# Performance work log

Measured on AMD Instinct MI355X. Metric: run time of the kernel, lower is better.

Reference implementation:

```python
import jax, jax.numpy as jnp
import numpy as np

D_MODEL = 1024
EXPAND = 2
HEADDIM = 64
D_STATE = 64
CHUNK = 64
D_INNER = EXPAND * D_MODEL          # 2048
NHEADS = D_INNER // HEADDIM         # 32
D_MLP = int(2.5 * D_MODEL)          # 2560
BATCH = 2
SEQLEN = 4096
PROJ = 2 * D_INNER + 2 * NHEADS * D_STATE + NHEADS + NHEADS * (D_STATE // 2)


def rmsnorm(x, w, eps=1e-5):
    return x * jax.lax.rsqrt(jnp.mean(x * x, axis=-1, keepdims=True) + eps) * w


def apply_rope(x, angles):
    x1 = x[..., 0::2]
    x2 = x[..., 1::2]
    c = jnp.cos(angles)
    s = jnp.sin(angles)
    ev = c * x1 - s * x2
    od = s * x1 + c * x2
    return jnp.stack([ev, od], axis=-1).reshape(x.shape)


def segsum(x):
    # x: (b,h,c,l) -> (b,h,c,l,l); [i,j] = sum_{j<k<=i} x_k (no -inf mask, as in source)
    T = x.shape[-1]
    xx = jnp.broadcast_to(x[..., :, None], x.shape + (T,))
    mask = jnp.tril(jnp.ones((T, T), dtype=bool), -1)
    xx = jnp.where(mask, xx, 0.0)
    return jnp.cumsum(xx, axis=-2)


def ssd(x, A, B, C, chunk):
    # x: (b,s,h,p), A: (b,s,h), B/C: (b,s,h,n); s % chunk == 0
    b, s, h, p = x.shape
    n = B.shape[-1]
    c = s // chunk
    x_c = x.reshape(b, c, chunk, h, p).transpose(0, 1, 3, 2, 4)  # (b,c,h,l,p)
    B_c = B.reshape(b, c, chunk, h, n).transpose(0, 1, 3, 2, 4)  # (b,c,h,l,n)
    C_c = C.reshape(b, c, chunk, h, n).transpose(0, 1, 3, 2, 4)
    A_c = A.reshape(b, c, chunk, h).transpose(0, 1, 3, 2)        # (b,c,h,l)
    A_cum = jnp.cumsum(A_c, axis=-1)
    L = jnp.exp(segsum(A_c.transpose(0, 2, 1, 3))).transpose(0, 2, 1, 3, 4)  # (b,c,h,l,l)
    Bx = jnp.einsum('bchln,bchlp->bchpn', B_c, x_c)
    Y_diag = jnp.einsum('bchln,bchls,bchpn->bchlp', C_c, L, Bx)
    decay_states = jnp.exp(A_cum[..., -1:] - A_cum)
    states = jnp.einsum('bchln,bchl,bchlp->bchpn', B_c, decay_states, x_c)  # (b,c,h,p,n)
    decay_chunk = jnp.exp(A_cum[..., -1])  # (b,c,h)
    h0 = jnp.zeros_like(states[:, 0])

    def step(carry, inp):
        dec, st = inp  # dec: (b,h), st: (b,h,p,n)
        carry = carry * dec[:, :, None, None] + st
        return carry, carry

    _, hs = jax.lax.scan(step, h0, (decay_chunk.transpose(1, 0, 2),
                                    states.transpose(1, 0, 2, 3, 4)))
    final_states = hs.transpose(1, 0, 2, 3, 4)  # (b,c,h,p,n)
    Y_off = jnp.einsum('bchln,bchpn,bchl->bchlp', C_c, final_states, jnp.exp(A_cum))
    Y = (Y_diag + Y_off).transpose(0, 1, 3, 2, 4).reshape(b, s, h * p)
    return Y


def setup_inputs() -> dict:
    key = jax.random.key(0)
    ks = jax.random.split(key, 12)
    sc = 0.02
    return {
        'x': jax.random.normal(ks[0], (BATCH, SEQLEN, D_MODEL), jnp.float32),
        'norm1_w': jnp.ones((D_MODEL,), jnp.float32),
        'norm2_w': jnp.ones((D_MODEL,), jnp.float32),
        'W_in': sc * jax.random.normal(ks[1], (D_MODEL, PROJ), jnp.float32),
        'W_out': sc * jax.random.normal(ks[2], (D_INNER, D_MODEL), jnp.float32),
        'A_log': jax.random.uniform(ks[3], (NHEADS,), jnp.float32, -4.0, -1.0),
        'D_param': jnp.ones((NHEADS,), jnp.float32),
        'dt_bias': jax.random.uniform(ks[4], (NHEADS,), jnp.float32, 0.001, 0.1),
        'B_bias': jnp.ones((1, NHEADS, D_STATE), jnp.float32),
        'C_bias': jnp.ones((1, NHEADS, D_STATE), jnp.float32),
        'Bn_w': jnp.ones((D_STATE,), jnp.float32),
        'Cn_w': jnp.ones((D_STATE,), jnp.float32),
        'Wg': sc * jax.random.normal(ks[5], (D_MODEL, D_MLP), jnp.float32),
        'Wu': sc * jax.random.normal(ks[6], (D_MODEL, D_MLP), jnp.float32),
        'Wd': sc * jax.random.normal(ks[7], (D_MLP, D_MODEL), jnp.float32),
    }


def reference(x, norm1_w, norm2_w, W_in, W_out, A_log, D_param, dt_bias,
              B_bias, C_bias, Bn_w, Cn_w, Wg, Wu, Wd):
    b, s, _ = x.shape
    h = rmsnorm(x, norm1_w)
    proj = h @ W_in
    i = 0
    z = proj[..., i:i + D_INNER]; i += D_INNER
    x_ssm = proj[..., i:i + D_INNER]; i += D_INNER
    B = proj[..., i:i + NHEADS * D_STATE].reshape(b, s, NHEADS, D_STATE); i += NHEADS * D_STATE
    C = proj[..., i:i + NHEADS * D_STATE].reshape(b, s, NHEADS, D_STATE); i += NHEADS * D_STATE
    dt = proj[..., i:i + NHEADS]; i += NHEADS
    theta = proj[..., i:].reshape(b, s, NHEADS, D_STATE // 2)
    dt = jax.nn.softplus(dt + dt_bias)                 # (b,s,h)
    A = -jnp.exp(A_log) * dt
    alpha = jnp.exp(A)
    gamma = (alpha - 1.0) / (A + 1e-6) * 0.5 + 1.0
    B = rmsnorm(B, Bn_w) + B_bias
    C = rmsnorm(C, Cn_w) + C_bias
    cum_theta = jnp.cumsum(dt[..., None] * theta, axis=1)
    B = apply_rope(B, cum_theta)
    C = apply_rope(C, cum_theta)
    x_ssm = x_ssm.reshape(b, s, NHEADS, HEADDIM)
    y = ssd(x_ssm * gamma[..., None], A, B, C, CHUNK)
    skip = jnp.broadcast_to((D_param * x_ssm.sum(-1))[..., None], x_ssm.shape)
    y = y + skip.reshape(b, s, -1)
    y = y * (z * jax.nn.sigmoid(z))
    y = y @ W_out
    x = x + y
    h2 = rmsnorm(x, norm2_w)
    g = h2 @ Wg
    x = x + ((g * jax.nn.sigmoid(g)) * (h2 @ Wu)) @ Wd
    return x
```

## Files before the change

kernel.cpp:

```cpp
#include <hip/hip_runtime.h>
#include <cstdint>
#include <cmath>


typedef __bf16 bf16;
typedef __bf16 bf16x2 __attribute__((ext_vector_type(2)));
typedef __bf16 bf16x4 __attribute__((ext_vector_type(4)));
typedef __bf16 bf16x8 __attribute__((ext_vector_type(8)));
typedef float fx4 __attribute__((ext_vector_type(4)));

#define DEV __device__ __forceinline__

#define OFF_PROJ    0ull
#define OFF_HHI     134217728ull
#define OFF_HLO     150994944ull
#define OFF_WTIN    167772160ull
#define OFF_WTHI    184549376ull
#define OFF_WTLO    186908672ull
#define OFF_PROJT   189267968ull
#define OFF_BX      189267968ull
#define OFF_STATES  222822400ull
#define OFF_WTOUT   222822400ull
#define OFF_WTGU    227016704ull
#define OFF_WTD     237502464ull
#define OFF_ABUF    256376832ull
#define OFF_XSUM    257425408ull
#define OFF_ROWSUM  258473984ull
#define OFF_EXPA    260571136ull
#define OFF_DCHUNK  262668288ull
#define OFF_GAMMA   262684672ull
#define WS_NEEDED   263733248ull

#define OFF_GU      0ull
#define OFF_MBF     83886080ull

DEV void async_copy16(void* lds, const void* gptr) {
  __builtin_amdgcn_global_load_lds(
      (const __attribute__((address_space(1))) unsigned int*)(gptr),
      (__attribute__((address_space(3))) unsigned int*)(lds),
      16, 0, 0);
}

DEV float warp_sum64(float v) {
  #pragma unroll
  for (int o = 32; o; o >>= 1) v += __shfl_xor(v, o);
  return v;
}

DEV float red16(float v) {
  v += __shfl_xor(v, 1); v += __shfl_xor(v, 2);
  v += __shfl_xor(v, 4); v += __shfl_xor(v, 8);
  return v;
}

DEV float softplus_f(float x) { return x > 20.f ? x : log1pf(expf(x)); }
DEV float sigmoid_f(float x) { return 1.f / (1.f + expf(-x)); }

__global__ __launch_bounds__(256) void transpose_cast(
    const float* __restrict__ src, int ld, int col0,
    bf16* __restrict__ dst, int R, int C)
{
  __shared__ float tile[32][33];
  const int c0 = blockIdx.x * 32, r0 = blockIdx.y * 32;
  const int tx = threadIdx.x & 31, ty = threadIdx.x >> 5;
  #pragma unroll
  for (int ii = 0; ii < 4; ++ii) {
    int i = ty + ii * 8;
    int c = c0 + tx;
    tile[i][tx] = (c < C) ? src[(size_t)(r0 + i) * ld + col0 + c] : 0.f;
  }
  __syncthreads();
  #pragma unroll
  for (int ii = 0; ii < 4; ++ii) {
    int i = ty + ii * 8;
    dst[(size_t)(c0 + i) * R + r0 + tx] = (bf16)tile[tx][i];
  }
}

__global__ __launch_bounds__(256) void transpose_cast_hilo(
    const float* __restrict__ src, int ld, int col0,
    bf16* __restrict__ dhi, bf16* __restrict__ dlo, int R, int C)
{
  __shared__ float tile[32][33];
  const int c0 = blockIdx.x * 32, r0 = blockIdx.y * 32;
  const int tx = threadIdx.x & 31, ty = threadIdx.x >> 5;
  #pragma unroll
  for (int ii = 0; ii < 4; ++ii) {
    int i = ty + ii * 8;
    int c = c0 + tx;
    tile[i][tx] = (c < C) ? src[(size_t)(r0 + i) * ld + col0 + c] : 0.f;
  }
  __syncthreads();
  #pragma unroll
  for (int ii = 0; ii < 4; ++ii) {
    int i = ty + ii * 8;
    float v = tile[tx][i];
    bf16 hi = (bf16)v;
    size_t o = (size_t)(c0 + i) * R + r0 + tx;
    dhi[o] = hi;
    dlo[o] = (bf16)(v - (float)hi);
  }
}

__global__ __launch_bounds__(256) void rmsnorm_kernel(
    const float* __restrict__ x, const float* __restrict__ w,
    bf16* __restrict__ hi, bf16* __restrict__ lo)
{
  __shared__ float red[4];
  const size_t row = blockIdx.x;
  const int tid = threadIdx.x;
  float4 v = ((const float4*)(x + row * 1024))[tid];
  float ss = v.x * v.x + v.y * v.y + v.z * v.z + v.w * v.w;
  ss = warp_sum64(ss);
  if ((tid & 63) == 0) red[tid >> 6] = ss;
  __syncthreads();
  float tot = red[0] + red[1] + red[2] + red[3];
  float s = rsqrtf(tot * (1.f / 1024.f) + 1e-5f);
  float4 wv = ((const float4*)w)[tid];
  float h0 = v.x * s * wv.x, h1 = v.y * s * wv.y, h2 = v.z * s * wv.z, h3 = v.w * s * wv.w;
  bf16x4 hv = { (bf16)h0, (bf16)h1, (bf16)h2, (bf16)h3 };
  *(bf16x4*)(hi + row * 1024 + tid * 4) = hv;
  if (lo) {
    bf16x4 lv = { (bf16)(h0 - (float)hv[0]), (bf16)(h1 - (float)hv[1]),
                  (bf16)(h2 - (float)hv[2]), (bf16)(h3 - (float)hv[3]) };
    *(bf16x4*)(lo + row * 1024 + tid * 4) = lv;
  }
}

template <int MODE>
__global__ __launch_bounds__(256) void gemm_bt(
    const bf16* A, const bf16* B, void* Cout, const float* resid,
    int K, int lda, int ldc)
{
  __shared__ bf16 As[128 * 64];
  __shared__ bf16 Bs[128 * 64];
  const int tid = threadIdx.x, wid = tid >> 6, lane = tid & 63;
  const int m0 = blockIdx.y * 128, n0 = blockIdx.x * 128;
  const int wm = (wid & 1) * 64, wn = (wid >> 1) * 64;
  fx4 acc[4][4];
  #pragma unroll
  for (int i = 0; i < 4; ++i)
    #pragma unroll
    for (int j = 0; j < 4; ++j) { fx4 z = {0.f, 0.f, 0.f, 0.f}; acc[i][j] = z; }

  const int srow = wid * 32 + (lane >> 3);
  const int slot = lane & 7;

  for (int k0 = 0; k0 < K; k0 += 64) {
    __syncthreads();
    #pragma unroll
    for (int i = 0; i < 4; ++i) {
      int m = srow + i * 8;
      int cA = ((slot ^ (m & 7)) * 8);
      async_copy16(&As[wid * 2048 + i * 512], A + (size_t)(m0 + m) * lda + k0 + cA);
    }
    #pragma unroll
    for (int i = 0; i < 4; ++i) {
      int n = srow + i * 8;
      int cB = ((slot ^ (n & 7)) * 8);
      async_copy16(&Bs[wid * 2048 + i * 512], B + (size_t)(n0 + n) * K + k0 + cB);
    }
    __syncthreads();
    #pragma unroll
    for (int kk = 0; kk < 2; ++kk) {
      bf16x8 af[4], bfr[4];
      #pragma unroll
      for (int i = 0; i < 4; ++i) {
        int mm = wm + i * 16 + (lane & 15);
        int sA = (kk * 4 + (lane >> 4)) ^ (mm & 7);
        af[i] = *(const bf16x8*)&As[mm * 64 + sA * 8];
        int nn = wn + i * 16 + (lane & 15);
        int sB = (kk * 4 + (lane >> 4)) ^ (nn & 7);
        bfr[i] = *(const bf16x8*)&Bs[nn * 64 + sB * 8];
      }
      #pragma unroll
      for (int i = 0; i < 4; ++i)
        #pragma unroll
        for (int j = 0; j < 4; ++j)
          acc[i][j] = __builtin_amdgcn_mfma_f32_16x16x32_bf16(af[i], bfr[j], acc[i][j], 0, 0, 0);
    }
  }
  const int r0 = (lane >> 4) * 4, cc = lane & 15;
  #pragma unroll
  for (int i = 0; i < 4; ++i) {
    #pragma unroll
    for (int j = 0; j < 4; ++j) {
      #pragma unroll
      for (int r = 0; r < 4; ++r) {
        int m = m0 + wm + i * 16 + r0 + r;
        int n = n0 + wn + j * 16 + cc;
        size_t off = (size_t)m * ldc + n;
        float v = acc[i][j][r];
        if (MODE == 1) ((bf16*)Cout)[off] = (bf16)v;
        else ((float*)Cout)[off] = v + resid[off];
      }
    }
  }
}

__global__ __launch_bounds__(256) void gemm_tail(
    const bf16* Ahi, const bf16* Alo, const bf16* Whi, const bf16* Wlo,
    float* Cout)
{
  __shared__ bf16 Ah[128 * 64], Al[128 * 64], Bh[128 * 64], Bl[128 * 64];
  const int tid = threadIdx.x, wid = tid >> 6, lane = tid & 63;
  const int m0 = blockIdx.y * 128, n0 = blockIdx.x * 128;
  const int wm = (wid & 1) * 64, wn = (wid >> 1) * 64;
  fx4 acc[4][4];
  #pragma unroll
  for (int i = 0; i < 4; ++i)
    #pragma unroll
    for (int j = 0; j < 4; ++j) { fx4 z = {0.f, 0.f, 0.f, 0.f}; acc[i][j] = z; }

  const int srow = wid * 32 + (lane >> 3);
  const int slot = lane & 7;

  for (int k0 = 0; k0 < 1024; k0 += 64) {
    __syncthreads();
    #pragma unroll
    for (int i = 0; i < 4; ++i) {
      int m = srow + i * 8;
      int cA = ((slot ^ (m & 7)) * 8);
      size_t ao = (size_t)(m0 + m) * 1024 + k0 + cA;
      async_copy16(&Ah[wid * 2048 + i * 512], Ahi + ao);
      async_copy16(&Al[wid * 2048 + i * 512], Alo + ao);
      int n = srow + i * 8;
      int cB = ((slot ^ (n & 7)) * 8);
      size_t bo = (size_t)(n0 + n) * 1024 + k0 + cB;
      async_copy16(&Bh[wid * 2048 + i * 512], Whi + bo);
      async_copy16(&Bl[wid * 2048 + i * 512], Wlo + bo);
    }
    __syncthreads();
    #pragma unroll
    for (int kk = 0; kk < 2; ++kk) {
      bf16x8 ah[4], al[4], bh[4], bl[4];
      #pragma unroll
      for (int i = 0; i < 4; ++i) {
        int mm = wm + i * 16 + (lane & 15);
        int sA = (kk * 4 + (lane >> 4)) ^ (mm & 7);
        ah[i] = *(const bf16x8*)&Ah[mm * 64 + sA * 8];
        al[i] = *(const bf16x8*)&Al[mm * 64 + sA * 8];
        int nn = wn + i * 16 + (lane & 15);
        int sB = (kk * 4 + (lane >> 4)) ^ (nn & 7);
        bh[i] = *(const bf16x8*)&Bh[nn * 64 + sB * 8];
        bl[i] = *(const bf16x8*)&Bl[nn * 64 + sB * 8];
      }
      #pragma unroll
      for (int i = 0; i < 4; ++i)
        #pragma unroll
        for (int j = 0; j < 4; ++j) {
          acc[i][j] = __builtin_amdgcn_mfma_f32_16x16x32_bf16(ah[i], bh[j], acc[i][j], 0, 0, 0);
          acc[i][j] = __builtin_amdgcn_mfma_f32_16x16x32_bf16(ah[i], bl[j], acc[i][j], 0, 0, 0);
          acc[i][j] = __builtin_amdgcn_mfma_f32_16x16x32_bf16(al[i], bh[j], acc[i][j], 0, 0, 0);
        }
    }
  }
  const int r0 = (lane >> 4) * 4, cc = lane & 15;
  #pragma unroll
  for (int i = 0; i < 4; ++i)
    #pragma unroll
    for (int j = 0; j < 4; ++j)
      #pragma unroll
      for (int r = 0; r < 4; ++r) {
        int m = m0 + wm + i * 16 + r0 + r;
        int n = n0 + wn + j * 16 + cc;
        Cout[(size_t)m * 1152 + n] = acc[i][j][r];
      }
}

__global__ __launch_bounds__(256) void dt_kernel(
    float* projT, const float* __restrict__ A_log, const float* __restrict__ dt_bias,
    float* __restrict__ a_buf, float* __restrict__ gamma_buf)
{
  const int idx = blockIdx.x * 256 + threadIdx.x;
  const int t = idx >> 5, h = idx & 31;
  float dtr = projT[(size_t)t * 1152 + h] + dt_bias[h];
  float dt = softplus_f(dtr);
  float a = -expf(A_log[h]) * dt;
  float alpha = expf(a);
  float gamma = (alpha - 1.f) / (a + 1e-6f) * 0.5f + 1.f;
  projT[(size_t)t * 1152 + h] = dt;
  a_buf[idx] = a;
  gamma_buf[idx] = gamma;
}

__global__ __launch_bounds__(256, 6) void gemm_proj(
    const bf16* A, const bf16* B, bf16* Cout,
    const float* __restrict__ gamma_buf, float* __restrict__ xsum,
    const float* __restrict__ Bn_w, const float* __restrict__ Cn_w,
    const float* __restrict__ B_bias, const float* __restrict__ C_bias)
{
  __shared__ bf16 As[128 * 64];
  __shared__ bf16 Bs[128 * 64];
  const int tid = threadIdx.x, wid = tid >> 6, lane = tid & 63;
  const int m0 = blockIdx.y * 128, n0 = blockIdx.x * 128;
  const int wm = (wid & 1) * 64, wn = (wid >> 1) * 64;
  fx4 acc[4][4];
  #pragma unroll
  for (int i = 0; i < 4; ++i)
    #pragma unroll
    for (int j = 0; j < 4; ++j) { fx4 z = {0.f, 0.f, 0.f, 0.f}; acc[i][j] = z; }

  const int srow = wid * 32 + (lane >> 3);
  const int slot = lane & 7;

  for (int k0 = 0; k0 < 1024; k0 += 64) {
    __syncthreads();
    #pragma unroll
    for (int i = 0; i < 4; ++i) {
      int m = srow + i * 8;
      int cA = ((slot ^ (m & 7)) * 8);
      async_copy16(&As[wid * 2048 + i * 512], A + (size_t)(m0 + m) * 1024 + k0 + cA);
    }
    #pragma unroll
    for (int i = 0; i < 4; ++i) {
      int n = srow + i * 8;
      int cB = ((slot ^ (n & 7)) * 8);
      async_copy16(&Bs[wid * 2048 + i * 512], B + (size_t)(n0 + n) * 1024 + k0 + cB);
    }
    __syncthreads();
    #pragma unroll
    for (int kk = 0; kk < 2; ++kk) {
      bf16x8 af[4], bfr[4];
      #pragma unroll
      for (int i = 0; i < 4; ++i) {
        int mm = wm + i * 16 + (lane & 15);
        int sA = (kk * 4 + (lane >> 4)) ^ (mm & 7);
        af[i] = *(const bf16x8*)&As[mm * 64 + sA * 8];
        int nn = wn + i * 16 + (lane & 15);
        int sB = (kk * 4 + (lane >> 4)) ^ (nn & 7);
        bfr[i] = *(const bf16x8*)&Bs[nn * 64 + sB * 8];
      }
      #pragma unroll
      for (int i = 0; i < 4; ++i)
        #pragma unroll
        for (int j = 0; j < 4; ++j)
          acc[i][j] = __builtin_amdgcn_mfma_f32_16x16x32_bf16(af[i], bfr[j], acc[i][j], 0, 0, 0);
    }
  }
  const int r0 = (lane >> 4) * 4, cc = lane & 15;
  const int reg = n0 >> 11;
  const int hh = ((n0 + wn) & 2047) >> 6;
  if (reg == 0) {
    #pragma unroll
    for (int i = 0; i < 4; ++i)
      #pragma unroll
      for (int j = 0; j < 4; ++j)
        #pragma unroll
        for (int r = 0; r < 4; ++r) {
          int m = m0 + wm + i * 16 + r0 + r;
          int n = n0 + wn + j * 16 + cc;
          Cout[(size_t)m * 8192 + n] = (bf16)acc[i][j][r];
        }
  } else if (reg == 1) {
    #pragma unroll
    for (int i = 0; i < 4; ++i)
      #pragma unroll
      for (int r = 0; r < 4; ++r) {
        float s = acc[i][0][r] + acc[i][1][r] + acc[i][2][r] + acc[i][3][r];
        s = red16(s);
        int m = m0 + wm + i * 16 + r0 + r;
        if (cc == 0) xsum[(size_t)m * 32 + hh] = s;
        float g = gamma_buf[(size_t)m * 32 + hh];
        #pragma unroll
        for (int j = 0; j < 4; ++j) {
          int n = n0 + wn + j * 16 + cc;
          Cout[(size_t)m * 8192 + n] = (bf16)(acc[i][j][r] * g);
        }
      }
  } else {
    const float* w = (reg == 2) ? Bn_w : Cn_w;
    const float* bias = (reg == 2) ? B_bias : C_bias;
    #pragma unroll
    for (int i = 0; i < 4; ++i)
      #pragma unroll
      for (int r = 0; r < 4; ++r) {
        float ss = acc[i][0][r] * acc[i][0][r] + acc[i][1][r] * acc[i][1][r]
                 + acc[i][2][r] * acc[i][2][r] + acc[i][3][r] * acc[i][3][r];
        ss = red16(ss);
        float sc = rsqrtf(ss * (1.f / 64.f) + 1e-5f);
        int m = m0 + wm + i * 16 + r0 + r;
        #pragma unroll
        for (int j = 0; j < 4; ++j) {
          int n = n0 + wn + j * 16 + cc;
          Cout[(size_t)m * 8192 + n] =
              (bf16)(acc[i][j][r] * sc * w[j * 16 + cc] + bias[hh * 64 + j * 16 + cc]);
        }
      }
  }
}

__global__ __launch_bounds__(256) void chunk_sum_kernel(
    const float* __restrict__ projT, float* __restrict__ S)
{
  __shared__ float lds[8 * 288];
  const int blk = blockIdx.x;
  const int hq = blockIdx.y;
  const size_t row0 = (size_t)blk * 64;
  const int tid = threadIdx.x;
  float s = 0.f;
  #pragma unroll 1
  for (int batch = 0; batch < 8; ++batch) {
    __syncthreads();
    const float* src = projT + (row0 + batch * 8) * 1152;
    #pragma unroll
    for (int i = 0; i < 9; ++i) {
      int idx = i * 256 + tid;
      int r = idx / 288, col = idx - r * 288;
      int gcol = (col < 32) ? col : (32 + hq * 256 + (col - 32));
      lds[idx] = src[r * 1152 + gcol];
    }
    __syncthreads();
    int hl = tid >> 5, d = tid & 31;
    #pragma unroll
    for (int r = 0; r < 8; ++r)
      s += lds[r * 288 + hq * 8 + hl] * lds[r * 288 + 32 + hl * 32 + d];
  }
  S[(size_t)blk * 1024 + hq * 256 + tid] = s;
}

__global__ __launch_bounds__(256) void rope_kernel(
    bf16* proj, const float* __restrict__ projT, const float* __restrict__ S)
{
  __shared__ float angs[64 * 33], angc[64 * 33];
  const int blk = blockIdx.x;
  const int b = blk >> 11, c = (blk >> 5) & 63, h = blk & 31;
  const size_t t0 = (size_t)b * 4096 + c * 64;
  const int w = threadIdx.x >> 6, lane = threadIdx.x & 63;
  const float* tr = projT + (t0 + lane) * 1152;
  float dtv = tr[h];
  const float* thp = tr + 32 + h * 32 + w * 8;
  float4 th0 = *(const float4*)thp;
  float4 th1 = *(const float4*)(thp + 4);
  const float* Sp = S + (size_t)(b * 64 + lane) * 1024 + h * 32 + w * 8;
  float4 S0 = *(const float4*)Sp;
  float4 S1 = *(const float4*)(Sp + 4);
  float th[8] = { th0.x, th0.y, th0.z, th0.w, th1.x, th1.y, th1.z, th1.w };
  float Sv[8] = { S0.x, S0.y, S0.z, S0.w, S1.x, S1.y, S1.z, S1.w };
  #pragma unroll 1
  for (int j = 0; j < 8; ++j) {
    int d = w * 8 + j;
    float sv = (lane < c) ? Sv[j] : 0.f;
    float off = warp_sum64(sv);
    float v = dtv * th[j];
    #pragma unroll
    for (int o = 1; o < 64; o <<= 1) { float u = __shfl_up(v, o); if (lane >= o) v += u; }
    float ang = off + v;
    float sn, cs;
    sincosf(ang, &sn, &cs);
    angs[lane * 33 + d] = sn;
    angc[lane * 33 + d] = cs;
  }
  __syncthreads();
  const int tt = threadIdx.x >> 2, q = threadIdx.x & 3;
  const size_t base = (t0 + tt) * 8192 + 4096 + h * 64 + q * 16;
  #pragma unroll
  for (int m = 0; m < 2; ++m) {
    bf16* p = proj + base + m * 2048;
    bf16x8 v0 = *(const bf16x8*)(p);
    bf16x8 v1 = *(const bf16x8*)(p + 8);
    bf16x8 r0, r1;
    #pragma unroll
    for (int pp = 0; pp < 4; ++pp) {
      int d = q * 8 + pp;
      float e1 = (float)v0[2 * pp], e2 = (float)v0[2 * pp + 1];
      float sn = angs[tt * 33 + d], cs = angc[tt * 33 + d];
      r0[2 * pp]     = (bf16)(cs * e1 - sn * e2);
      r0[2 * pp + 1] = (bf16)(sn * e1 + cs * e2);
    }
    #pragma unroll
    for (int pp = 0; pp < 4; ++pp) {
      int d = q * 8 + 4 + pp;
      float e1 = (float)v1[2 * pp], e2 = (float)v1[2 * pp + 1];
      float sn = angs[tt * 33 + d], cs = angc[tt * 33 + d];
      r1[2 * pp]     = (bf16)(cs * e1 - sn * e2);
      r1[2 * pp + 1] = (bf16)(sn * e1 + cs * e2);
    }
    *(bf16x8*)(p) = r0;
    *(bf16x8*)(p + 8) = r1;
  }
}

__global__ __launch_bounds__(256) void ssd1_kernel(
    const bf16* __restrict__ proj, const float* __restrict__ a_buf,
    bf16* __restrict__ Bx, bf16* __restrict__ states,
    float* __restrict__ rowsum, float* __restrict__ expac, float* __restrict__ dchunk)
{
  __shared__ bf16 Xs[64 * 72], Bs[64 * 72];
  __shared__ float acum[64], dsv[64];
  const int blk = blockIdx.x;
  const int h = blk & 31;
  const size_t bs0 = ((size_t)(blk >> 5)) * 64;
  const int tid = threadIdx.x;
  const int l = tid >> 2, p0 = (tid & 3) * 16;
  {
    const bf16* xrow = proj + (bs0 + l) * 8192 + 2048 + h * 64 + p0;
    *(bf16x8*)&Xs[l * 72 + p0]     = ((const bf16x8*)xrow)[0];
    *(bf16x8*)&Xs[l * 72 + p0 + 8] = ((const bf16x8*)xrow)[1];
    const bf16* brow = proj + (bs0 + l) * 8192 + 4096 + h * 64 + p0;
    *(bf16x8*)&Bs[l * 72 + p0]     = ((const bf16x8*)brow)[0];
    *(bf16x8*)&Bs[l * 72 + p0 + 8] = ((const bf16x8*)brow)[1];
  }
  if (tid < 64) {
    float v = a_buf[(bs0 + tid) * 32 + h];
    #pragma unroll
    for (int o = 1; o < 64; o <<= 1) { float u = __shfl_up(v, o); if (tid >= o) v += u; }
    acum[tid] = v;
    float a63 = __shfl(v, 63);
    dsv[tid] = expf(a63 - v);
    expac[(size_t)blk * 64 + tid] = expf(v);
    if (tid == 63) dchunk[blk] = expf(v);
  }
  __syncthreads();
  {
    float al = acum[l];
    float rs = 0.f;
    for (int s = tid & 3; s <= l; s += 4) rs += expf(al - acum[s]);
    rs += __shfl_xor(rs, 1);
    rs += __shfl_xor(rs, 2);
    if ((tid & 3) == 0) rowsum[(size_t)blk * 64 + l] = rs + (float)(63 - l);
  }
  const int wv = tid >> 6, lane = tid & 63;
  const int mi = lane & 15, kq = lane >> 4;
  const int m0 = wv * 16;
  fx4 accB[4], accS[4];
  #pragma unroll
  for (int j4 = 0; j4 < 4; ++j4) { fx4 z = {0.f,0.f,0.f,0.f}; accB[j4] = z; accS[j4] = z; }
  #pragma unroll
  for (int kk = 0; kk < 2; ++kk) {
    const int lb = kk * 32 + kq * 8;
    bf16x8 aX, aXd;
    #pragma unroll
    for (int j = 0; j < 8; ++j) {
      bf16 xv = Xs[(lb + j) * 72 + m0 + mi];
      aX[j] = xv;
      aXd[j] = (bf16)((float)xv * dsv[lb + j]);
    }
    #pragma unroll
    for (int j4 = 0; j4 < 4; ++j4) {
      bf16x8 bB;
      #pragma unroll
      for (int j = 0; j < 8; ++j) bB[j] = Bs[(lb + j) * 72 + j4 * 16 + mi];
      accB[j4] = __builtin_amdgcn_mfma_f32_16x16x32_bf16(aX, bB, accB[j4], 0, 0, 0);
      accS[j4] = __builtin_amdgcn_mfma_f32_16x16x32_bf16(aXd, bB, accS[j4], 0, 0, 0);
    }
  }
  const size_t obase = (size_t)blk * 4096;
  #pragma unroll
  for (int j4 = 0; j4 < 4; ++j4) {
    #pragma unroll
    for (int r = 0; r < 4; ++r) {
      int p = m0 + kq * 4 + r;
      int n = j4 * 16 + mi;
      Bx[obase + p * 64 + n] = (bf16)accB[j4][r];
      states[obase + p * 64 + n] = (bf16)accS[j4][r];
    }
  }
}

__global__ __launch_bounds__(128) void ssd2_kernel(
    bf16* __restrict__ states, const float* __restrict__ dchunk)
{
  const int blk = blockIdx.x;
  const int b = blk >> 9, rest = blk & 511;
  const int h = rest >> 4, q = rest & 15;
  const int e0 = q * 256 + threadIdx.x * 2;
  float fs0 = 0.f, fs1 = 0.f;
  #pragma unroll 2
  for (int c = 0; c < 64; ++c) {
    size_t idx = ((size_t)(b * 2048 + c * 32 + h) * 4096) + e0;
    float dec = dchunk[b * 2048 + c * 32 + h];
    bf16x2 st = *(const bf16x2*)(states + idx);
    fs0 = fs0 * dec + (float)st[0];
    fs1 = fs1 * dec + (float)st[1];
    bf16x2 o = { (bf16)fs0, (bf16)fs1 };
    *(bf16x2*)(states + idx) = o;
  }
}

__global__ __launch_bounds__(256) void ssd3_kernel(
    bf16* proj, const bf16* __restrict__ Bx, const bf16* __restrict__ FS,
    const float* __restrict__ rowsum, const float* __restrict__ expac,
    const float* __restrict__ xsum, const float* __restrict__ D_param)
{
  __shared__ bf16 Cs[64 * 72], BxS[64 * 72], FSs[64 * 72];
  __shared__ float rs_s[64], ea_s[64], sk_s[64];
  const int blk = blockIdx.x;
  const int h = blk & 31;
  const size_t bs0 = ((size_t)(blk >> 5)) * 64;
  const int tid = threadIdx.x;
  const int l = tid >> 2, q0 = (tid & 3) * 16;
  {
    const bf16* crow = proj + (bs0 + l) * 8192 + 6144 + h * 64 + q0;
    *(bf16x8*)&Cs[l * 72 + q0]     = ((const bf16x8*)crow)[0];
    *(bf16x8*)&Cs[l * 72 + q0 + 8] = ((const bf16x8*)crow)[1];
    size_t mb = (size_t)blk * 4096 + l * 64 + q0;
    *(bf16x8*)&BxS[l * 72 + q0]     = ((const bf16x8*)(Bx + mb))[0];
    *(bf16x8*)&BxS[l * 72 + q0 + 8] = ((const bf16x8*)(Bx + mb))[1];
    *(bf16x8*)&FSs[l * 72 + q0]     = ((const bf16x8*)(FS + mb))[0];
    *(bf16x8*)&FSs[l * 72 + q0 + 8] = ((const bf16x8*)(FS + mb))[1];
  }
  if (tid < 64) {
    rs_s[tid] = rowsum[(size_t)blk * 64 + tid];
    ea_s[tid] = expac[(size_t)blk * 64 + tid];
    sk_s[tid] = D_param[h] * xsum[(bs0 + tid) * 32 + h];
  }
  __syncthreads();
  const int wv = tid >> 6, lane = tid & 63;
  const int mi = lane & 15, kq = lane >> 4;
  const int m0 = wv * 16;
  fx4 acc1[4], acc2[4];
  #pragma unroll
  for (int j4 = 0; j4 < 4; ++j4) { fx4 z = {0.f,0.f,0.f,0.f}; acc1[j4] = z; acc2[j4] = z; }
  #pragma unroll
  for (int kk = 0; kk < 2; ++kk) {
    bf16x8 aC = *(const bf16x8*)&Cs[(m0 + mi) * 72 + kk * 32 + kq * 8];
    #pragma unroll
    for (int j4 = 0; j4 < 4; ++j4) {
      bf16x8 bx = *(const bf16x8*)&BxS[(j4 * 16 + mi) * 72 + kk * 32 + kq * 8];
      bf16x8 fs = *(const bf16x8*)&FSs[(j4 * 16 + mi) * 72 + kk * 32 + kq * 8];
      acc1[j4] = __builtin_amdgcn_mfma_f32_16x16x32_bf16(aC, bx, acc1[j4], 0, 0, 0);
      acc2[j4] = __builtin_amdgcn_mfma_f32_16x16x32_bf16(aC, fs, acc2[j4], 0, 0, 0);
    }
  }
  #pragma unroll
  for (int j4 = 0; j4 < 4; ++j4) {
    #pragma unroll
    for (int r = 0; r < 4; ++r) {
      int li = m0 + kq * 4 + r;
      int p = j4 * 16 + mi;
      float y = rs_s[li] * acc1[j4][r] + ea_s[li] * acc2[j4][r] + sk_s[li];
      size_t zoff = (bs0 + li) * 8192 + h * 64 + p;
      float z = (float)proj[zoff];
      proj[zoff + 2048] = (bf16)(y * z * sigmoid_f(z));
    }
  }
}

__global__ __launch_bounds__(256) void silu_mul_kernel(
    const bf16* __restrict__ gu, bf16* __restrict__ m)
{
  const size_t row = blockIdx.y;
  const int col2 = blockIdx.x * 256 + threadIdx.x;
  const size_t gi = row * 5120 + col2 * 2;
  bf16x2 g = *(const bf16x2*)(gu + gi);
  bf16x2 u = *(const bf16x2*)(gu + gi + 2560);
  float g0 = (float)g[0], g1 = (float)g[1];
  float m0 = g0 * sigmoid_f(g0) * (float)u[0];
  float m1 = g1 * sigmoid_f(g1) * (float)u[1];
  bf16x2 mv = { (bf16)m0, (bf16)m1 };
  *(bf16x2*)(m + row * 2560 + col2 * 2) = mv;
}

extern "C" void kernel_launch(void* const* d_in, const int* in_sizes, int n_in,
                              void* d_out, int out_size, void* d_ws, size_t ws_size,
                              hipStream_t stream) {
  (void)in_sizes; (void)n_in; (void)out_size;
  if (ws_size < WS_NEEDED) return;
  const float* x       = (const float*)d_in[0];
  const float* n1w     = (const float*)d_in[1];
  const float* n2w     = (const float*)d_in[2];
  const float* W_in    = (const float*)d_in[3];
  const float* W_out   = (const float*)d_in[4];
  const float* A_log   = (const float*)d_in[5];
  const float* D_param = (const float*)d_in[6];
  const float* dt_bias = (const float*)d_in[7];
  const float* B_bias  = (const float*)d_in[8];
  const float* C_bias  = (const float*)d_in[9];
  const float* Bn_w    = (const float*)d_in[10];
  const float* Cn_w    = (const float*)d_in[11];
  const float* Wg      = (const float*)d_in[12];
  const float* Wu      = (const float*)d_in[13];
  const float* Wd      = (const float*)d_in[14];
  float* out = (float*)d_out;
  char* ws = (char*)d_ws;

  bf16*  proj   = (bf16*)(ws + OFF_PROJ);
  float* projT  = (float*)(ws + OFF_PROJT);
  bf16*  h_hi   = (bf16*)(ws + OFF_HHI);
  bf16*  h_lo   = (bf16*)(ws + OFF_HLO);
  bf16*  Wt_in  = (bf16*)(ws + OFF_WTIN);
  bf16*  Wt_hi  = (bf16*)(ws + OFF_WTHI);
  bf16*  Wt_lo  = (bf16*)(ws + OFF_WTLO);
  bf16*  Wt_out = (bf16*)(ws + OFF_WTOUT);
  bf16*  Wt_gu  = (bf16*)(ws + OFF_WTGU);
  bf16*  Wt_d   = (bf16*)(ws + OFF_WTD);
  bf16*  Bx     = (bf16*)(ws + OFF_BX);
  bf16*  states = (bf16*)(ws + OFF_STATES);
  float* a_buf  = (float*)(ws + OFF_ABUF);
  float* xsum_  = (float*)(ws + OFF_XSUM);
  float* rowsum = (float*)(ws + OFF_ROWSUM);
  float* expac  = (float*)(ws + OFF_EXPA);
  float* dchunk = (float*)(ws + OFF_DCHUNK);
  float* gamma_ = (float*)(ws + OFF_GAMMA);
  float* Ssum   = (float*)(ws + OFF_HLO);
  bf16*  ybf    = proj + 2048;
  bf16*  gubf   = (bf16*)(ws + OFF_GU);
  bf16*  mbf    = (bf16*)(ws + OFF_MBF);
  bf16*  h2bf   = h_hi;
  float* x2     = out;

  transpose_cast<<<dim3(256, 32), 256, 0, stream>>>(W_in, 9248, 0, Wt_in, 1024, 8192);
  transpose_cast_hilo<<<dim3(36, 32), 256, 0, stream>>>(W_in, 9248, 8192, Wt_hi, Wt_lo, 1024, 1056);

  rmsnorm_kernel<<<8192, 256, 0, stream>>>(x, n1w, h_hi, h_lo);

  gemm_tail<<<dim3(9, 64), 256, 0, stream>>>(h_hi, h_lo, Wt_hi, Wt_lo, projT);
  dt_kernel<<<1024, 256, 0, stream>>>(projT, A_log, dt_bias, a_buf, gamma_);
  gemm_proj<<<dim3(64, 64), 256, 0, stream>>>(h_hi, Wt_in, proj, gamma_, xsum_,
                                              Bn_w, Cn_w, B_bias, C_bias);

  chunk_sum_kernel<<<dim3(128, 4), 256, 0, stream>>>(projT, Ssum);
  rope_kernel<<<4096, 256, 0, stream>>>(proj, projT, Ssum);

  ssd1_kernel<<<4096, 256, 0, stream>>>(proj, a_buf, Bx, states, rowsum, expac, dchunk);
  ssd2_kernel<<<1024, 128, 0, stream>>>(states, dchunk);
  ssd3_kernel<<<4096, 256, 0, stream>>>(proj, Bx, states, rowsum, expac, xsum_, D_param);

  transpose_cast<<<dim3(32, 64), 256, 0, stream>>>(W_out, 1024, 0, Wt_out, 2048, 1024);
  transpose_cast<<<dim3(80, 32), 256, 0, stream>>>(Wg, 2560, 0, Wt_gu, 1024, 2560);
  transpose_cast<<<dim3(80, 32), 256, 0, stream>>>(Wu, 2560, 0, Wt_gu + (size_t)2560 * 1024, 1024, 2560);
  transpose_cast<<<dim3(32, 80), 256, 0, stream>>>(Wd, 1024, 0, Wt_d, 2560, 1024);

  gemm_bt<2><<<dim3(8, 64), 256, 0, stream>>>(ybf, Wt_out, x2, x, 2048, 8192, 1024);

  rmsnorm_kernel<<<8192, 256, 0, stream>>>(x2, n2w, h2bf, nullptr);
  gemm_bt<1><<<dim3(40, 64), 256, 0, stream>>>(h2bf, Wt_gu, gubf, nullptr, 1024, 1024, 5120);
  silu_mul_kernel<<<dim3(5, 8192), 256, 0, stream>>>(gubf, mbf);
  gemm_bt<2><<<dim3(8, 64), 256, 0, stream>>>(mbf, Wt_d, out, x2, 2560, 2560, 1024);
}
```

Before: 862.4 us.

## Rewrite input projection GEMM with 256x256 tiles and double-buffered async pipeline

Replaces the 128x128 projection GEMM with a 512-thread, 256x256-tile kernel that double-buffers K slices in 128KB of LDS. Global loads for later stages are issued while MFMAs run, using explicit vmcnt waits, barriers and setprio. Blocks are remapped with an XCD-style swizzle for L2 locality. The larger tile raises arithmetic intensity and hides load latency, at the cost of lower occupancy, higher register pressure, and fewer blocks for load balance.

After: 812.9 us. 5.7% less time.

```diff
diff --git a/kernel.cpp b/kernel.cpp
--- a/kernel.cpp
+++ b/kernel.cpp
@@ -284,87 +284,123 @@
   gamma_buf[idx] = gamma;
 }
 
-__global__ __launch_bounds__(256, 6) void gemm_proj(
-    const bf16* A, const bf16* B, bf16* Cout,
+__global__ __launch_bounds__(512, 2) void gemm_proj256(
+    const bf16* __restrict__ A, const bf16* __restrict__ B, bf16* __restrict__ Cout,
     const float* __restrict__ gamma_buf, float* __restrict__ xsum,
     const float* __restrict__ Bn_w, const float* __restrict__ Cn_w,
     const float* __restrict__ B_bias, const float* __restrict__ C_bias)
 {
-  __shared__ bf16 As[128 * 64];
-  __shared__ bf16 Bs[128 * 64];
+  __shared__ bf16 lds[65536];
   const int tid = threadIdx.x, wid = tid >> 6, lane = tid & 63;
-  const int m0 = blockIdx.y * 128, n0 = blockIdx.x * 128;
-  const int wm = (wid & 1) * 64, wn = (wid >> 1) * 64;
-  fx4 acc[4][4];
-  #pragma unroll
-  for (int i = 0; i < 4; ++i)
+  const int bid = blockIdx.x;
+  const int swz = (bid & 7) * 128 + (bid >> 3);
+  const int by = swz >> 5, bx = swz & 31;
+  const int m0 = by * 256, n0 = bx * 256;
+  const int wr = wid >> 2, wc = wid & 3;
+  const int fl = lane & 15, fq = lane >> 4;
+  const int rloc = wid * 8 + (lane >> 3);
+  const int colSwz = ((lane & 7) ^ (lane >> 3)) * 8;
+
+  fx4 acc[8][4];
+  #pragma unroll
+  for (int i = 0; i < 8; ++i)
     #pragma unroll
     for (int j = 0; j < 4; ++j) { fx4 z = {0.f, 0.f, 0.f, 0.f}; acc[i][j] = z; }
 
-  const int srow = wid * 32 + (lane >> 3);
-  const int slot = lane & 7;
-
-  for (int k0 = 0; k0 < 1024; k0 += 64) {
-    __syncthreads();
-    #pragma unroll
-    for (int i = 0; i < 4; ++i) {
-      int m = srow + i * 8;
-      int cA = ((slot ^ (m & 7)) * 8);
-      async_copy16(&As[wid * 2048 + i * 512], A + (size_t)(m0 + m) * 1024 + k0 + cA);
-    }
-    #pragma unroll
-    for (int i = 0; i < 4; ++i) {
-      int n = srow + i * 8;
-      int cB = ((slot ^ (n & 7)) * 8);
-      async_copy16(&Bs[wid * 2048 + i * 512], B + (size_t)(n0 + n) * 1024 + k0 + cB);
-    }
-    __syncthreads();
-    #pragma unroll
-    for (int kk = 0; kk < 2; ++kk) {
-      bf16x8 af[4], bfr[4];
-      #pragma unroll
-      for (int i = 0; i < 4; ++i) {
-        int mm = wm + i * 16 + (lane & 15);
-        int sA = (kk * 4 + (lane >> 4)) ^ (mm & 7);
-        af[i] = *(const bf16x8*)&As[mm * 64 + sA * 8];
-        int nn = wn + i * 16 + (lane & 15);
-        int sB = (kk * 4 + (lane >> 4)) ^ (nn & 7);
-        bfr[i] = *(const bf16x8*)&Bs[nn * 64 + sB * 8];
-      }
-      #pragma unroll
-      for (int i = 0; i < 4; ++i)
+  const bf16* gA = A + (size_t)(m0 + rloc) * 1024 + colSwz;
+  const bf16* gB = B + (size_t)(n0 + rloc) * 1024 + colSwz;
+
+  auto STAGE = [&](int u, int h) {
+    const bf16* s = (h < 2) ? gB : gA;
+    s += (size_t)(h & 1) * 128 * 1024 + u * 64;
+    bf16* d = &lds[((u & 1) * 4 + h) * 8192 + wid * 512];
+    async_copy16(d, s);
+    async_copy16(d + 4096, s + 64 * 1024);
+  };
+
+  STAGE(0, 0); STAGE(0, 1); STAGE(0, 2); STAGE(0, 3);
+  STAGE(1, 0); STAGE(1, 1);
+  asm volatile("s_waitcnt vmcnt(4)" ::: "memory");
+  __builtin_amdgcn_s_barrier();
+
+  const int NT = 16;
+  bf16x8 bfrag[4][2];
+  for (int t = 0; t < NT; ++t) {
+    const int Bb = (t & 1) * 32768;
+    const int Ab = Bb + 16384;
+    #pragma unroll
+    for (int p = 0; p < 4; ++p) {
+      bf16x8 af[2][2];
+      if (p == 0) {
+        #pragma unroll
+        for (int j = 0; j < 4; ++j) {
+          int nn = wc * 64 + j * 16 + fl;
+          #pragma unroll
+          for (int kk = 0; kk < 2; ++kk) {
+            int q = (kk * 4 + fq) ^ (nn & 7);
+            bfrag[j][kk] = *(const bf16x8*)&lds[Bb + nn * 64 + q * 8];
+          }
+        }
+      }
+      #pragma unroll
+      for (int ii = 0; ii < 2; ++ii) {
+        int mm = wr * 128 + (p * 2 + ii) * 16 + fl;
+        #pragma unroll
+        for (int kk = 0; kk < 2; ++kk) {
+          int q = (kk * 4 + fq) ^ (mm & 7);
+          af[ii][kk] = *(const bf16x8*)&lds[Ab + mm * 64 + q * 8];
+        }
+      }
+      {
+        int H = 4 * t + 6 + p;
+        if (H < 4 * NT) STAGE(H >> 2, H & 3);
+      }
+      if (p == 3) asm volatile("s_waitcnt vmcnt(4)" ::: "memory");
+      __builtin_amdgcn_s_barrier();
+      asm volatile("s_waitcnt lgkmcnt(0)" ::: "memory");
+      __builtin_amdgcn_sched_barrier(0);
+      __builtin_amdgcn_s_setprio(1);
+      #pragma unroll
+      for (int ii = 0; ii < 2; ++ii)
         #pragma unroll
         for (int j = 0; j < 4; ++j)
-          acc[i][j] = __builtin_amdgcn_mfma_f32_16x16x32_bf16(af[i], bfr[j], acc[i][j], 0, 0, 0);
-    }
-  }
-  const int r0 = (lane >> 4) * 4, cc = lane & 15;
-  const int reg = n0 >> 11;
-  const int hh = ((n0 + wn) & 2047) >> 6;
+          #pragma unroll
+          for (int kk = 0; kk < 2; ++kk)
+            acc[p * 2 + ii][j] = __builtin_amdgcn_mfma_f32_16x16x32_bf16(
+                af[ii][kk], bfrag[j][kk], acc[p * 2 + ii][j], 0, 0, 0);
+      __builtin_amdgcn_s_setprio(0);
+      __builtin_amdgcn_s_barrier();
+    }
+  }
+
+  const int reg = bx >> 3;
+  const int hh = ((n0 + wc * 64) & 2047) >> 6;
+  const int mwb = m0 + wr * 128;
+  const int nwb = n0 + wc * 64;
   if (reg == 0) {
     #pragma unroll
-    for (int i = 0; i < 4; ++i)
+    for (int i = 0; i < 8; ++i)
       #pragma unroll
       for (int j = 0; j < 4; ++j)
         #pragma unroll
         for (int r = 0; r < 4; ++r) {
-          int m = m0 + wm + i * 16 + r0 + r;
-          int n = n0 + wn + j * 16 + cc;
+          int m = mwb + i * 16 + fq * 4 + r;
+          int n = nwb + j * 16 + fl;
           Cout[(size_t)m * 8192 + n] = (bf16)acc[i][j][r];
         }
   } else if (reg == 1) {
     #pragma unroll
-    for (int i = 0; i < 4; ++i)
+    for (int i = 0; i < 8; ++i)
       #pragma unroll
       for (int r = 0; r < 4; ++r) {
         float s = acc[i][0][r] + acc[i][1][r] + acc[i][2][r] + acc[i][3][r];
         s = red16(s);
-        int m = m0 + wm + i * 16 + r0 + r;
-        if (cc == 0) xsum[(size_t)m * 32 + hh] = s;
+        int m = mwb + i * 16 + fq * 4 + r;
+        if (fl == 0) xsum[(size_t)m * 32 + hh] = s;
         float g = gamma_buf[(size_t)m * 32 + hh];
         #pragma unroll
         for (int j = 0; j < 4; ++j) {
-          int n = n0 + wn + j * 16 + cc;
+          int n = nwb + j * 16 + fl;
           Cout[(size_t)m * 8192 + n] = (bf16)(acc[i][j][r] * g);
         }
       }
@@ -372,19 +408,19 @@
     const float* w = (reg == 2) ? Bn_w : Cn_w;
     const float* bias = (reg == 2) ? B_bias : C_bias;
     #pragma unroll
-    for (int i = 0; i < 4; ++i)
+    for (int i = 0; i < 8; ++i)
       #pragma unroll
       for (int r = 0; r < 4; ++r) {
         float ss = acc[i][0][r] * acc[i][0][r] + acc[i][1][r] * acc[i][1][r]
                  + acc[i][2][r] * acc[i][2][r] + acc[i][3][r] * acc[i][3][r];
         ss = red16(ss);
         float sc = rsqrtf(ss * (1.f / 64.f) + 1e-5f);
-        int m = m0 + wm + i * 16 + r0 + r;
+        int m = mwb + i * 16 + fq * 4 + r;
         #pragma unroll
         for (int j = 0; j < 4; ++j) {
-          int n = n0 + wn + j * 16 + cc;
-          Cout[(size_t)m * 8192 + n] =
-              (bf16)(acc[i][j][r] * sc * w[j * 16 + cc] + bias[hh * 64 + j * 16 + cc]);
+          int c = j * 16 + fl;
+          Cout[(size_t)m * 8192 + nwb + c] =
+              (bf16)(acc[i][j][r] * sc * w[c] + bias[hh * 64 + c]);
         }
       }
   }
@@ -707,8 +743,8 @@
 
   gemm_tail<<<dim3(9, 64), 256, 0, stream>>>(h_hi, h_lo, Wt_hi, Wt_lo, projT);
   dt_kernel<<<1024, 256, 0, stream>>>(projT, A_log, dt_bias, a_buf, gamma_);
-  gemm_proj<<<dim3(64, 64), 256, 0, stream>>>(h_hi, Wt_in, proj, gamma_, xsum_,
-                                              Bn_w, Cn_w, B_bias, C_bias);
+  gemm_proj256<<<dim3(1024), 512, 0, stream>>>(h_hi, Wt_in, proj, gamma_, xsum_,
+                                               Bn_w, Cn_w, B_bias, C_bias);
 
   chunk_sum_kernel<<<dim3(128, 4), 256, 0, stream>>>(projT, Ssum);
   rope_kernel<<<4096, 256, 0, stream>>>(proj, projT, Ssum);
```
